# Optimization experiments

Hardware: AMD Instinct MI355X
Metric: run time of the kernel (lower is better)

## Reference

```python
import jax, jax.numpy as jnp
import numpy as np

N_STATE = 2048
N_HEAD = 16
HEAD_DIM = N_STATE // N_HEAD  # 128
ROPE_THETA = 10000.0


def setup_inputs() -> dict:
    key = jax.random.key(0)
    ks = jax.random.split(key, 8)
    B, S, D = 2, 2048, N_STATE
    scale = 1.0 / np.sqrt(D)
    x = jax.random.normal(ks[0], (B, S, D), dtype=jnp.float32)
    Wq = jax.random.normal(ks[1], (D, D), dtype=jnp.float32) * scale
    bq = jnp.zeros((D,), dtype=jnp.float32)
    Wk = jax.random.normal(ks[2], (D, D), dtype=jnp.float32) * scale  # key has no bias
    Wv = jax.random.normal(ks[3], (D, D), dtype=jnp.float32) * scale
    bv = jnp.zeros((D,), dtype=jnp.float32)
    Wo = jax.random.normal(ks[4], (D, D), dtype=jnp.float32) * scale
    bo = jnp.zeros((D,), dtype=jnp.float32)
    return {"x": x, "Wq": Wq, "bq": bq, "Wk": Wk, "Wv": Wv, "bv": bv, "Wo": Wo, "bo": bo}


def _rope(t, pos):
    # t: [B, S, H, hd]; torchtune-style interleaved rotary (pairs of adjacent dims)
    hd = t.shape[-1]
    inv_freq = 1.0 / (ROPE_THETA ** (jnp.arange(0, hd, 2, dtype=jnp.float32) / hd))  # [hd/2]
    ang = pos[:, None] * inv_freq[None, :]                    # [S, hd/2]
    cos = jnp.cos(ang)[None, :, None, :].astype(t.dtype)       # [1,S,1,hd/2]
    sin = jnp.sin(ang)[None, :, None, :].astype(t.dtype)
    t1 = t[..., 0::2]
    t2 = t[..., 1::2]
    rot = jnp.stack([t1 * cos - t2 * sin, t2 * cos + t1 * sin], axis=-1)
    return rot.reshape(t.shape)


def reference(x, Wq, bq, Wk, Wv, bv, Wo, bo):
    B, S, D = x.shape
    H, hd = N_HEAD, D // N_HEAD
    q = (x @ Wq.T + bq).reshape(B, S, H, hd)
    k = (x @ Wk.T).reshape(B, S, H, hd)
    v = (x @ Wv.T + bv).reshape(B, S, H, hd)
    pos = jnp.arange(S, dtype=jnp.float32)
    q = _rope(q, pos)
    k = _rope(k, pos)
    # [B,H,S,hd]
    q = q.transpose(0, 2, 1, 3)
    k = k.transpose(0, 2, 1, 3)
    v = v.transpose(0, 2, 1, 3)
    scale = 1.0 / jnp.sqrt(jnp.asarray(hd, dtype=x.dtype))
    scores = jnp.einsum('bhqd,bhkd->bhqk', q, k) * scale       # [B,H,S,S]
    causal = jnp.tril(jnp.ones((S, S), dtype=bool))
    scores = jnp.where(causal[None, None], scores, jnp.finfo(scores.dtype).min)
    probs = jax.nn.softmax(scores, axis=-1)
    a = jnp.einsum('bhqk,bhkd->bhqd', probs, v)                # [B,H,S,hd]
    a = a.transpose(0, 2, 1, 3).reshape(B, S, D)
    return a @ Wo.T + bo
```

## Files before the change

kernel.cpp:

```cpp
#include <hip/hip_runtime.h>
#include <stdint.h>

typedef float f32x4 __attribute__((ext_vector_type(4)));
typedef __bf16 bf16x8 __attribute__((ext_vector_type(8)));
typedef unsigned short us8 __attribute__((ext_vector_type(8)));
typedef unsigned short us4 __attribute__((ext_vector_type(4)));
typedef unsigned int u32;

#define MFMA16(A, B, C) __builtin_amdgcn_mfma_f32_16x16x32_bf16( \
    __builtin_bit_cast(bf16x8, (A)), __builtin_bit_cast(bf16x8, (B)), (C), 0, 0, 0)

__device__ __forceinline__ unsigned short f2bf(float f) {
  u32 u = __builtin_bit_cast(u32, f);
  u = u + 0x7fffu + ((u >> 16) & 1u);
  return (unsigned short)(u >> 16);
}
__device__ __forceinline__ float bf2f(unsigned short b) {
  u32 u = ((u32)b) << 16;
  return __builtin_bit_cast(float, u);
}
__device__ __forceinline__ void gload16(const void* g, void* lds) {
  __builtin_amdgcn_global_load_lds((const __attribute__((address_space(1))) u32*)g,
                                   (__attribute__((address_space(3))) u32*)lds, 16, 0, 0);
}

__global__ __launch_bounds__(256) void convert_all(
    const float* __restrict__ x, const float* __restrict__ wq, const float* __restrict__ wk,
    const float* __restrict__ wv, const float* __restrict__ wo,
    unsigned short* __restrict__ xb, unsigned short* __restrict__ wcat,
    unsigned short* __restrict__ wob, float2* __restrict__ tab) {
  if (blockIdx.x >= 2048) {
    int t0 = ((int)blockIdx.x - 2048) * 2048 + (int)threadIdx.x * 8;
#pragma unroll
    for (int j = 0; j < 8; ++j) {
      int idx = t0 + j;
      int s = idx >> 6, i = idx & 63;
      float ang = (float)s * exp2f(-(float)i * 0.2076205059304703f);
      float sv, cv;
      sincosf(ang, &sv, &cv);
      tab[idx] = make_float2(cv, sv);
    }
    return;
  }
  int tid = blockIdx.x * 256 + threadIdx.x;
  int nth = 2048 * 256;
  const float* srcs[5] = {x, wq, wk, wv, wo};
  unsigned short* dsts[5] = {xb, wcat, wcat + 4194304, wcat + 8388608, wob};
  const int n4s[5] = {2097152, 1048576, 1048576, 1048576, 1048576};
#pragma unroll
  for (int sg = 0; sg < 5; ++sg) {
    const float4* s = (const float4*)srcs[sg];
    us4* d = (us4*)dsts[sg];
    int n4 = n4s[sg];
    for (int i = tid; i < n4; i += nth) {
      float4 v = s[i];
      us4 o;
      o[0] = f2bf(v.x); o[1] = f2bf(v.y); o[2] = f2bf(v.z); o[3] = f2bf(v.w);
      d[i] = o;
    }
  }
}

template <int EPI>
__global__ __launch_bounds__(512, 2) void gemmsw(
    const unsigned short* __restrict__ A, const unsigned short* __restrict__ B,
    int nTN, int N,
    float* __restrict__ outF, const float* __restrict__ bias,
    unsigned short* __restrict__ qb, unsigned short* __restrict__ kb,
    unsigned short* __restrict__ vtb, const float* __restrict__ bq,
    const float* __restrict__ bv, const float2* __restrict__ tab) {
  constexpr int KT = 32;
  __shared__ alignas(16) char L[131072];
  char* Lp = L;
  int bid = (int)blockIdx.x, nwg = (int)gridDim.x;
  {
    int qq = nwg >> 3;
    int xcd = bid & 7, idx = bid >> 3;
    bid = xcd * qq + idx;
  }
  int tm = bid / nTN, tn = bid % nTN;
  int t = (int)threadIdx.x, l = t & 63, w = t >> 6;
  int g = l >> 4, ln = l & 15;
  int wr = w >> 2, wc = w & 3;
  int lr = l >> 3, lc = l & 7;
  int scol = lc ^ lr;
  const unsigned short* pAs = A + (size_t)(tm * 256 + w * 8 + lr) * 2048 + scol * 8;
  const unsigned short* pBs = B + (size_t)(tn * 256 + w * 8 + lr) * 2048 + scol * 8;

  f32x4 acc[2][2][4][2] = {};
  us8 af[4][2], bf[2][2][2];

#define FENCE asm volatile("" ::: "memory")
#define BAR do { FENCE; __builtin_amdgcn_s_barrier(); FENCE; } while (0)
#define VMW_(n) asm volatile("s_waitcnt vmcnt(" #n ")" ::: "memory")
#define VMW(n) VMW_(n)
#define STA(i, kt, bufsel) do { if ((kt) < KT)                                \
    gload16(pAs + (size_t)(i) * 131072 + (size_t)(kt) * 64,                   \
            Lp + (bufsel) * 65536 + (i) * 8192 + w * 1024); } while (0)
#define STB(i, kt, bufsel) do { if ((kt) < KT)                                \
    gload16(pBs + (size_t)(i) * 131072 + (size_t)(kt) * 64,                   \
            Lp + (bufsel) * 65536 + 32768 + (i) * 8192 + w * 1024); } while (0)
#define RD_A(mh_, bufsel) do {                                                \
    _Pragma("unroll") for (int mf = 0; mf < 4; ++mf)                          \
    _Pragma("unroll") for (int kc = 0; kc < 2; ++kc)                          \
      af[mf][kc] = *(const us8*)(Lp + (bufsel) * 65536 +                      \
          (wr * 128 + (mh_) * 64 + mf * 16 + ln) * 128 +                      \
          ((kc * 64 + g * 16) ^ ((ln & 7) << 4)));                            \
  } while (0)
#define RD_B(nh_, bufsel) do {                                                \
    _Pragma("unroll") for (int nf = 0; nf < 2; ++nf)                          \
    _Pragma("unroll") for (int kc = 0; kc < 2; ++kc)                          \
      bf[nh_][nf][kc] = *(const us8*)(Lp + (bufsel) * 65536 + 32768 +         \
          (wc * 64 + (nh_) * 32 + nf * 16 + ln) * 128 +                       \
          ((kc * 64 + g * 16) ^ ((ln & 7) << 4)));                            \
  } while (0)
#define MM(mh_, nh_) do {                                                     \
    __builtin_amdgcn_s_setprio(1);                                            \
    _Pragma("unroll") for (int mf = 0; mf < 4; ++mf)                          \
    _Pragma("unroll") for (int nf = 0; nf < 2; ++nf)                          \
    _Pragma("unroll") for (int kc = 0; kc < 2; ++kc)                          \
      acc[mh_][nh_][mf][nf] = MFMA16(af[mf][kc], bf[nh_][nf][kc],             \
                                     acc[mh_][nh_][mf][nf]);                  \
    __builtin_amdgcn_s_setprio(0);                                            \
  } while (0)
#define TILE(kt, b, VM0, VM1, VM3) do {                                       \
   RD_A(0, b); RD_B(0, b);                                             \
          STB(0, (kt) + 1, (b) ^ 1); STB(1, (kt) + 1, (b) ^ 1);               \
          BAR; MM(0, 0); VMW(VM0); BAR;                                       \
   RD_B(1, b);                                                         \
          STA(0, (kt) + 1, (b) ^ 1); STA(2, (kt) + 1, (b) ^ 1);               \
          BAR; MM(0, 1); VMW(VM1); BAR;                                       \
   RD_A(1, b);                                                         \
          STB(2, (kt) + 1, (b) ^ 1); STB(3, (kt) + 1, (b) ^ 1);               \
          BAR; MM(1, 0); BAR;                                                 \
   STA(1, (kt) + 1, (b) ^ 1); STA(3, (kt) + 1, (b) ^ 1);               \
          MM(1, 1); VMW(VM3); BAR;                                            \
} while (0)

  STB(0, 0, 0); STB(1, 0, 0); STA(0, 0, 0); STA(2, 0, 0);
  STB(2, 0, 0); STB(3, 0, 0); STA(1, 0, 0); STA(3, 0, 0);
  VMW(4); BAR;

#pragma unroll 1
  for (int kt = 0; kt < 30; kt += 2) {
    TILE(kt, 0, 4, 4, 4);
    TILE(kt + 1, 1, 4, 4, 4);
  }
  TILE(30, 0, 4, 4, 4);
  TILE(31, 1, 2, 0, 0);

#undef TILE
#undef MM
#undef RD_B
#undef RD_A
#undef STB
#undef STA
#undef VMW
#undef VMW_
#undef BAR
#undef FENCE

  if (EPI == 1) {
#pragma unroll
    for (int mh = 0; mh < 2; ++mh)
#pragma unroll
    for (int nh = 0; nh < 2; ++nh)
#pragma unroll
    for (int mf = 0; mf < 4; ++mf)
#pragma unroll
    for (int nf = 0; nf < 2; ++nf) {
      int n = tn * 256 + wc * 64 + nh * 32 + nf * 16 + ln;
      float bz = bias[n];
      int m0 = tm * 256 + wr * 128 + mh * 64 + mf * 16 + g * 4;
#pragma unroll
      for (int r = 0; r < 4; ++r)
        outF[(size_t)(m0 + r) * N + n] = acc[mh][nh][mf][nf][r] + bz;
    }
  } else {
#pragma unroll
    for (int mh = 0; mh < 2; ++mh)
#pragma unroll
    for (int nh = 0; nh < 2; ++nh)
#pragma unroll
    for (int mf = 0; mf < 4; ++mf)
#pragma unroll
    for (int nf = 0; nf < 2; ++nf) {
      int n6 = tn * 256 + wc * 64 + nh * 32 + nf * 16 + ln;
      int sel = n6 >> 11, d = n6 & 2047, h = d >> 7, hd = d & 127;
      int m0 = tm * 256 + wr * 128 + mh * 64 + mf * 16 + g * 4;
      int b = m0 >> 11, s0 = m0 & 2047;
      if (sel == 2) {
        float badd = bv[d];
        us4 pk;
#pragma unroll
        for (int r = 0; r < 4; ++r) pk[r] = f2bf(acc[mh][nh][mf][nf][r] + badd);
        *(us4*)&vtb[((size_t)(b * 16 + h) * 128 + hd) * 2048 + s0] = pk;
      } else {
        unsigned short* dst = sel ? kb : qb;
        float badd = sel ? 0.f : bq[d];
        int odd = hd & 1;
#pragma unroll
        for (int r = 0; r < 4; ++r) {
          float val = acc[mh][nh][mf][nf][r] + badd;
          float pv = __shfl_xor(val, 1);
          float2 cs = tab[((s0 + r) << 6) | (hd >> 1)];
          float rot = odd ? (val * cs.x + pv * cs.y) : (val * cs.x - pv * cs.y);
          dst[((size_t)(b * 16 + h) * 2048 + (s0 + r)) * 128 + hd] = f2bf(rot);
        }
      }
    }
  }
}

template <int EPI>
__global__ __launch_bounds__(512, 2) void gemm2(
    const unsigned short* __restrict__ A, const unsigned short* __restrict__ B,
    int nTN, int N,
    float* __restrict__ outF, const float* __restrict__ bias) {
  constexpr int K = 2048, KT = 64;
  __shared__ alignas(16) char L[4 * 24576];
  int bid = (int)blockIdx.x, nwg = (int)gridDim.x;
  {
    int qq = nwg >> 3;
    int xcd = bid & 7, idx = bid >> 3;
    bid = xcd * qq + idx;
  }
  int tm = bid / nTN, tn = bid % nTN;
  int t = (int)threadIdx.x, l = t & 63, w = t >> 6;
  int g = l >> 4, ln = l & 15;
  int wr = w >> 2, wc = w & 3;
  const unsigned short* Ab =
      A + (size_t)(tm * 128 + w * 16 + (l >> 2)) * K + (((l & 3) ^ ((l >> 4) & 3))) * 8;
  const unsigned short* Bb =
      B + (size_t)(tn * 256 + w * 16 + (l >> 2)) * K + (((l & 3) ^ ((l >> 4) & 3))) * 8;
  f32x4 acc[4][4] = {};

#define STAGE(tile) do {                                                      \
    char* Lb = L + ((tile) & 3) * 24576 + w * 1024;                           \
    int kc = (tile) * 32;                                                     \
    gload16(Ab + kc, Lb);                                                     \
    gload16(Bb + kc, Lb + 8192);                                              \
    gload16(Bb + (size_t)128 * K + kc, Lb + 16384);                           \
  } while (0)

#define GITER(kt, VM) do {                                                    \
    asm volatile("s_waitcnt vmcnt(" #VM ")" ::: "memory");                    \
    __builtin_amdgcn_s_barrier();                                             \
    __builtin_amdgcn_sched_barrier(0);                                        \
    asm volatile("" ::: "memory");                                            \
    if ((kt) + 3 < KT) STAGE((kt) + 3);                                       \
    const unsigned short* Lc = (const unsigned short*)(L + ((kt) & 3) * 24576); \
    us8 af[4], bfr[4];                                                        \
    _Pragma("unroll") for (int mf = 0; mf < 4; ++mf)                          \
      af[mf] = *(const us8*)&Lc[(wr * 64 + mf * 16 + ln) * 32 +               \
                                ((g ^ ((ln >> 2) & 3)) * 8)];                 \
    _Pragma("unroll") for (int nf = 0; nf < 4; ++nf)                          \
      bfr[nf] = *(const us8*)&Lc[4096 + (wc * 64 + nf * 16 + ln) * 32 +       \
                                 ((g ^ ((ln >> 2) & 3)) * 8)];                \
    __builtin_amdgcn_s_setprio(1);                                            \
    _Pragma("unroll") for (int mf = 0; mf < 4; ++mf)                          \
      _Pragma("unroll") for (int nf = 0; nf < 4; ++nf)                        \
        acc[mf][nf] = MFMA16(af[mf], bfr[nf], acc[mf][nf]);                   \
    __builtin_amdgcn_s_setprio(0);                                            \
  } while (0)

  STAGE(0); STAGE(1); STAGE(2);
#pragma unroll 1
  for (int kt = 0; kt < KT - 2; ++kt) GITER(kt, 6);
  GITER(KT - 2, 3);
  GITER(KT - 1, 0);
#undef STAGE
#undef GITER

#pragma unroll
  for (int mf = 0; mf < 4; ++mf)
#pragma unroll
    for (int nf = 0; nf < 4; ++nf) {
      int n = tn * 256 + wc * 64 + nf * 16 + ln;
      float bz = bias[n];
#pragma unroll
      for (int r = 0; r < 4; ++r) {
        int m = tm * 128 + wr * 64 + mf * 16 + g * 4 + r;
        outF[(size_t)m * N + n] = acc[mf][nf][r] + bz;
      }
    }
}

__global__ __launch_bounds__(512) void attn_k(
    const unsigned short* __restrict__ qg, const unsigned short* __restrict__ kg,
    const unsigned short* __restrict__ vtg, unsigned short* __restrict__ ab) {
  __shared__ alignas(16) unsigned short Kl[64 * 128];
  __shared__ alignas(16) unsigned short Vl[128 * 64];
  __shared__ alignas(16) unsigned short Pl[8][16 * 72];
  int bh = (int)blockIdx.x & 31;
  int pr = (int)blockIdx.x >> 5;
  int t = (int)threadIdx.x, l = t & 63, w = t >> 6;
  int g = l >> 4, ln = l & 15;
  int b = bh >> 4, h = bh & 15;
  const size_t bq0 = (size_t)bh * 2048 * 128;

#pragma unroll 1
  for (int half = 0; half < 2; ++half) {
    int qt = half ? 15 - pr : pr;
    int qbase = qt * 128;
    int qrow = qbase + w * 16 + ln;
    us8 qf[4];
#pragma unroll
    for (int kf = 0; kf < 4; ++kf)
      qf[kf] = *(const us8*)&qg[bq0 + (size_t)qrow * 128 + kf * 32 + g * 8];
    f32x4 o[8] = {};
    float mrow = -1e30f, lrow = 0.f;
    int nkt = (qbase >> 6) + 2;
#pragma unroll 1
    for (int kt = 0; kt < nkt; ++kt) {
      __syncthreads();
#pragma unroll
      for (int i = 0; i < 2; ++i) {
        int fb = i * 8192 + w * 1024;
        int flat = fb + l * 16;
        int row = flat >> 8, colb = flat & 255;
        int sc = colb ^ ((row & 7) << 4);
        gload16(kg + (bq0 + (size_t)(kt * 64 + row) * 128 + (sc >> 1)), (char*)Kl + fb);
        int rv = flat >> 7, cv2 = flat & 127;
        int scv = cv2 ^ ((rv & 7) << 4);
        gload16(vtg + (bq0 + (size_t)rv * 2048 + kt * 64 + (scv >> 1)), (char*)Vl + fb);
      }
      __syncthreads();
      f32x4 st[4];
#pragma unroll
      for (int kfr = 0; kfr < 4; ++kfr) {
        f32x4 acc = {};
        int row = kfr * 16 + ln;
        int swz = (row & 7) << 4;
#pragma unroll
        for (int kf = 0; kf < 4; ++kf) {
          us8 kfrag = *(const us8*)((const char*)Kl + row * 256 + ((kf * 64 + g * 16) ^ swz));
          acc = MFMA16(kfrag, qf[kf], acc);
        }
        st[kfr] = acc;
      }
      float pmax = -1e30f;
#pragma unroll
      for (int kfr = 0; kfr < 4; ++kfr)
#pragma unroll
        for (int r = 0; r < 4; ++r) {
          int key = kt * 64 + kfr * 16 + g * 4 + r;
          float sv = key <= qrow ? st[kfr][r] * 0.08838834764831845f : -1e30f;
          st[kfr][r] = sv;
          pmax = fmaxf(pmax, sv);
        }
      pmax = fmaxf(pmax, __shfl_xor(pmax, 16));
      pmax = fmaxf(pmax, __shfl_xor(pmax, 32));
      if (__ballot(pmax > mrow + 8.f)) {
        float mnew = pmax > mrow + 8.f ? pmax : mrow;
        float corr = exp2f((mrow - mnew) * 1.44269504f);
        mrow = mnew;
        lrow *= corr;
#pragma unroll
        for (int r = 0; r < 4; ++r) {
          float cr = __shfl(corr, g * 4 + r);
#pragma unroll
          for (int nf = 0; nf < 8; ++nf) o[nf][r] *= cr;
        }
      }
      float lsum = 0.f;
#pragma unroll
      for (int kfr = 0; kfr < 4; ++kfr) {
        us4 pk;
#pragma unroll
        for (int r = 0; r < 4; ++r) {
          float p = exp2f((st[kfr][r] - mrow) * 1.44269504f);
          lsum += p;
          pk[r] = f2bf(p);
        }
        *(us4*)&Pl[w][ln * 72 + kfr * 16 + g * 4] = pk;
      }
      lsum += __shfl_xor(lsum, 16);
      lsum += __shfl_xor(lsum, 32);
      lrow += lsum;
#pragma unroll
      for (int kf2 = 0; kf2 < 2; ++kf2) {
        us8 pa = *(const us8*)&Pl[w][ln * 72 + kf2 * 32 + g * 8];
#pragma unroll
        for (int nf = 0; nf < 8; ++nf) {
          int row = nf * 16 + ln;
          us8 vb = *(const us8*)((const char*)Vl + row * 128 +
                                 ((kf2 * 64 + g * 16) ^ ((row & 7) << 4)));
          o[nf] = MFMA16(pa, vb, o[nf]);
        }
      }
    }
    float invl = 1.f / lrow;
#pragma unroll
    for (int r = 0; r < 4; ++r) {
      float ir = __shfl(invl, g * 4 + r);
      int srow = qbase + w * 16 + g * 4 + r;
      size_t base = ((size_t)b * 2048 + srow) * 2048 + h * 128 + ln;
#pragma unroll
      for (int nf = 0; nf < 8; ++nf) ab[base + (size_t)nf * 16] = f2bf(o[nf][r] * ir);
    }
  }
}

extern "C" void kernel_launch(void* const* d_in, const int* in_sizes, int n_in,
                              void* d_out, int out_size, void* d_ws, size_t ws_size,
                              hipStream_t stream) {
  const float* x  = (const float*)d_in[0];
  const float* Wq = (const float*)d_in[1];
  const float* bq = (const float*)d_in[2];
  const float* Wk = (const float*)d_in[3];
  const float* Wv = (const float*)d_in[4];
  const float* bv = (const float*)d_in[5];
  const float* Wo = (const float*)d_in[6];
  const float* bo = (const float*)d_in[7];
  float* out = (float*)d_out;

  unsigned short* ws = (unsigned short*)d_ws;
  unsigned short* xb   = ws;
  unsigned short* wcat = xb + 8388608;
  unsigned short* wob  = wcat + 12582912;
  unsigned short* qb   = wob + 4194304;
  unsigned short* kb   = qb + 8388608;
  unsigned short* vtb  = kb + 8388608;
  float2* tab = (float2*)(vtb + 8388608);

  convert_all<<<2112, 256, 0, stream>>>(x, Wq, Wk, Wv, Wo, xb, wcat, wob, tab);
  gemmsw<0><<<384, 512, 0, stream>>>(xb, wcat, 24, 6144,
                                     nullptr, nullptr, qb, kb, vtb, bq, bv, tab);
  attn_k<<<256, 512, 0, stream>>>(qb, kb, vtb, xb );
  gemm2<1><<<256, 512, 0, stream>>>(xb, wob, 8, 2048, out, bo);
}
```

Before: 267.0 us.

## Process paired query tiles together sharing double-buffered K/V tiles in attention

The attention kernel now handles its two causal query tiles (the early and the late one) in the same key loop instead of one after the other. Each K/V tile staged in LDS is used by both tiles, so the shared prefix of keys is loaded only once. K/V staging is also double-buffered: the next tile is prefetched while the current one is computed, which leaves one barrier per iteration instead of two. In exchange, two sets of output accumulators and Q fragments stay live, which raises register pressure and risks spills at 512 threads per block, and the LDS footprint grows.

```diff
diff --git a/kernel.cpp b/kernel.cpp
--- a/kernel.cpp
+++ b/kernel.cpp
@@ -289,8 +289,8 @@
 __global__ __launch_bounds__(512) void attn_k(
     const unsigned short* __restrict__ qg, const unsigned short* __restrict__ kg,
     const unsigned short* __restrict__ vtg, unsigned short* __restrict__ ab) {
-  __shared__ alignas(16) unsigned short Kl[64 * 128];
-  __shared__ alignas(16) unsigned short Vl[128 * 64];
+  __shared__ alignas(16) unsigned short Kl[2][64 * 128];
+  __shared__ alignas(16) unsigned short Vl[2][128 * 64];
   __shared__ alignas(16) unsigned short Pl[8][16 * 72];
   int bh = (int)blockIdx.x & 31;
   int pr = (int)blockIdx.x >> 5;
@@ -299,105 +299,123 @@
   int b = bh >> 4, h = bh & 15;
   const size_t bq0 = (size_t)bh * 2048 * 128;
 
+  const int qbA = pr * 128, qbB = (15 - pr) * 128;
+  const int qrowA = qbA + w * 16 + ln, qrowB = qbB + w * 16 + ln;
+  us8 qfA[4], qfB[4];
+#pragma unroll
+  for (int kf = 0; kf < 4; ++kf) {
+    qfA[kf] = *(const us8*)&qg[bq0 + (size_t)qrowA * 128 + kf * 32 + g * 8];
+    qfB[kf] = *(const us8*)&qg[bq0 + (size_t)qrowB * 128 + kf * 32 + g * 8];
+  }
+  f32x4 oA[8] = {}, oB[8] = {};
+  float mA = -1e30f, lA = 0.f, mB = -1e30f, lB = 0.f;
+  const int nktA = (qbA >> 6) + 2;
+  const int nkt  = (qbB >> 6) + 2;
+
+#define STAGEKV(kt1, bsel) do {                                               \
+    _Pragma("unroll") for (int i = 0; i < 2; ++i) {                           \
+      int fb = i * 8192 + w * 1024;                                           \
+      int flat = fb + l * 16;                                                 \
+      int row = flat >> 8, colb = flat & 255;                                 \
+      int sc = colb ^ ((row & 7) << 4);                                       \
+      gload16(kg + (bq0 + (size_t)((kt1) * 64 + row) * 128 + (sc >> 1)),      \
+              (char*)Kl + (bsel) * 16384 + fb);                               \
+      int rv = flat >> 7, cv2 = flat & 127;                                   \
+      int scv = cv2 ^ ((rv & 7) << 4);                                        \
+      gload16(vtg + (bq0 + (size_t)rv * 2048 + (kt1) * 64 + (scv >> 1)),      \
+              (char*)Vl + (bsel) * 16384 + fb);                               \
+    }                                                                         \
+  } while (0)
+
+#define COMPUTE(qf, o, mrow, lrow, qrow, kt, bo) do {                         \
+    f32x4 st[4];                                                              \
+    _Pragma("unroll") for (int kfr = 0; kfr < 4; ++kfr) {                     \
+      f32x4 acc = {};                                                         \
+      int row = kfr * 16 + ln;                                                \
+      int swz = (row & 7) << 4;                                               \
+      _Pragma("unroll") for (int kf = 0; kf < 4; ++kf) {                      \
+        us8 kfrag = *(const us8*)((const char*)Kl + (bo) + row * 256 +        \
+                                  ((kf * 64 + g * 16) ^ swz));                \
+        acc = MFMA16(kfrag, qf[kf], acc);                                     \
+      }                                                                       \
+      st[kfr] = acc;                                                          \
+    }                                                                         \
+    float pmax = -1e30f;                                                      \
+    _Pragma("unroll") for (int kfr = 0; kfr < 4; ++kfr)                       \
+    _Pragma("unroll") for (int r = 0; r < 4; ++r) {                           \
+      int key = (kt) * 64 + kfr * 16 + g * 4 + r;                             \
+      float sv = key <= (qrow) ? st[kfr][r] * 0.08838834764831845f : -1e30f;  \
+      st[kfr][r] = sv;                                                        \
+      pmax = fmaxf(pmax, sv);                                                 \
+    }                                                                         \
+    pmax = fmaxf(pmax, __shfl_xor(pmax, 16));                                 \
+    pmax = fmaxf(pmax, __shfl_xor(pmax, 32));                                 \
+    if (__ballot(pmax > (mrow) + 8.f)) {                                      \
+      float mnew = pmax > (mrow) + 8.f ? pmax : (mrow);                       \
+      float corr = exp2f(((mrow) - mnew) * 1.44269504f);                      \
+      (mrow) = mnew;                                                          \
+      (lrow) *= corr;                                                         \
+      _Pragma("unroll") for (int r = 0; r < 4; ++r) {                         \
+        float cr = __shfl(corr, g * 4 + r);                                   \
+        _Pragma("unroll") for (int nf = 0; nf < 8; ++nf) o[nf][r] *= cr;      \
+      }                                                                       \
+    }                                                                         \
+    float lsum = 0.f;                                                         \
+    _Pragma("unroll") for (int kfr = 0; kfr < 4; ++kfr) {                     \
+      us4 pk;                                                                 \
+      _Pragma("unroll") for (int r = 0; r < 4; ++r) {                         \
+        float p = exp2f((st[kfr][r] - (mrow)) * 1.44269504f);                 \
+        lsum += p;                                                            \
+        pk[r] = f2bf(p);                                                      \
+      }                                                                       \
+      *(us4*)&Pl[w][ln * 72 + kfr * 16 + g * 4] = pk;                         \
+    }                                                                         \
+    lsum += __shfl_xor(lsum, 16);                                             \
+    lsum += __shfl_xor(lsum, 32);                                             \
+    (lrow) += lsum;                                                           \
+    _Pragma("unroll") for (int kf2 = 0; kf2 < 2; ++kf2) {                     \
+      us8 pa = *(const us8*)&Pl[w][ln * 72 + kf2 * 32 + g * 8];               \
+      _Pragma("unroll") for (int nf = 0; nf < 8; ++nf) {                      \
+        int row = nf * 16 + ln;                                               \
+        us8 vb = *(const us8*)((const char*)Vl + (bo) + row * 128 +           \
+                               ((kf2 * 64 + g * 16) ^ ((row & 7) << 4)));     \
+        o[nf] = MFMA16(pa, vb, o[nf]);                                        \
+      }                                                                       \
+    }                                                                         \
+  } while (0)
+
+  STAGEKV(0, 0);
 #pragma unroll 1
-  for (int half = 0; half < 2; ++half) {
-    int qt = half ? 15 - pr : pr;
-    int qbase = qt * 128;
-    int qrow = qbase + w * 16 + ln;
-    us8 qf[4];
-#pragma unroll
-    for (int kf = 0; kf < 4; ++kf)
-      qf[kf] = *(const us8*)&qg[bq0 + (size_t)qrow * 128 + kf * 32 + g * 8];
-    f32x4 o[8] = {};
-    float mrow = -1e30f, lrow = 0.f;
-    int nkt = (qbase >> 6) + 2;
-#pragma unroll 1
-    for (int kt = 0; kt < nkt; ++kt) {
-      __syncthreads();
-#pragma unroll
-      for (int i = 0; i < 2; ++i) {
-        int fb = i * 8192 + w * 1024;
-        int flat = fb + l * 16;
-        int row = flat >> 8, colb = flat & 255;
-        int sc = colb ^ ((row & 7) << 4);
-        gload16(kg + (bq0 + (size_t)(kt * 64 + row) * 128 + (sc >> 1)), (char*)Kl + fb);
-        int rv = flat >> 7, cv2 = flat & 127;
-        int scv = cv2 ^ ((rv & 7) << 4);
-        gload16(vtg + (bq0 + (size_t)rv * 2048 + kt * 64 + (scv >> 1)), (char*)Vl + fb);
-      }
-      __syncthreads();
-      f32x4 st[4];
-#pragma unroll
-      for (int kfr = 0; kfr < 4; ++kfr) {
-        f32x4 acc = {};
-        int row = kfr * 16 + ln;
-        int swz = (row & 7) << 4;
-#pragma unroll
-        for (int kf = 0; kf < 4; ++kf) {
-          us8 kfrag = *(const us8*)((const char*)Kl + row * 256 + ((kf * 64 + g * 16) ^ swz));
-          acc = MFMA16(kfrag, qf[kf], acc);
-        }
-        st[kfr] = acc;
-      }
-      float pmax = -1e30f;
-#pragma unroll
-      for (int kfr = 0; kfr < 4; ++kfr)
-#pragma unroll
-        for (int r = 0; r < 4; ++r) {
-          int key = kt * 64 + kfr * 16 + g * 4 + r;
-          float sv = key <= qrow ? st[kfr][r] * 0.08838834764831845f : -1e30f;
-          st[kfr][r] = sv;
-          pmax = fmaxf(pmax, sv);
-        }
-      pmax = fmaxf(pmax, __shfl_xor(pmax, 16));
-      pmax = fmaxf(pmax, __shfl_xor(pmax, 32));
-      if (__ballot(pmax > mrow + 8.f)) {
-        float mnew = pmax > mrow + 8.f ? pmax : mrow;
-        float corr = exp2f((mrow - mnew) * 1.44269504f);
-        mrow = mnew;
-        lrow *= corr;
-#pragma unroll
-        for (int r = 0; r < 4; ++r) {
-          float cr = __shfl(corr, g * 4 + r);
-#pragma unroll
-          for (int nf = 0; nf < 8; ++nf) o[nf][r] *= cr;
-        }
-      }
-      float lsum = 0.f;
-#pragma unroll
-      for (int kfr = 0; kfr < 4; ++kfr) {
-        us4 pk;
-#pragma unroll
-        for (int r = 0; r < 4; ++r) {
-          float p = exp2f((st[kfr][r] - mrow) * 1.44269504f);
-          lsum += p;
-          pk[r] = f2bf(p);
-        }
-        *(us4*)&Pl[w][ln * 72 + kfr * 16 + g * 4] = pk;
-      }
-      lsum += __shfl_xor(lsum, 16);
-      lsum += __shfl_xor(lsum, 32);
-      lrow += lsum;
-#pragma unroll
-      for (int kf2 = 0; kf2 < 2; ++kf2) {
-        us8 pa = *(const us8*)&Pl[w][ln * 72 + kf2 * 32 + g * 8];
-#pragma unroll
-        for (int nf = 0; nf < 8; ++nf) {
-          int row = nf * 16 + ln;
-          us8 vb = *(const us8*)((const char*)Vl + row * 128 +
-                                 ((kf2 * 64 + g * 16) ^ ((row & 7) << 4)));
-          o[nf] = MFMA16(pa, vb, o[nf]);
-        }
-      }
-    }
-    float invl = 1.f / lrow;
+  for (int kt = 0; kt < nkt; ++kt) {
+    __syncthreads();
+    if (kt + 1 < nkt) STAGEKV(kt + 1, (kt + 1) & 1);
+    int bo = (kt & 1) * 16384;
+    COMPUTE(qfB, oB, mB, lB, qrowB, kt, bo);
+    if (kt < nktA) COMPUTE(qfA, oA, mA, lA, qrowA, kt, bo);
+  }
+#undef COMPUTE
+#undef STAGEKV
+
+  {
+    float invl = 1.f / lB;
 #pragma unroll
     for (int r = 0; r < 4; ++r) {
       float ir = __shfl(invl, g * 4 + r);
-      int srow = qbase + w * 16 + g * 4 + r;
+      int srow = qbB + w * 16 + g * 4 + r;
       size_t base = ((size_t)b * 2048 + srow) * 2048 + h * 128 + ln;
 #pragma unroll
-      for (int nf = 0; nf < 8; ++nf) ab[base + (size_t)nf * 16] = f2bf(o[nf][r] * ir);
+      for (int nf = 0; nf < 8; ++nf) ab[base + (size_t)nf * 16] = f2bf(oB[nf][r] * ir);
+    }
+  }
+  {
+    float invl = 1.f / lA;
+#pragma unroll
+    for (int r = 0; r < 4; ++r) {
+      float ir = __shfl(invl, g * 4 + r);
+      int srow = qbA + w * 16 + g * 4 + r;
+      size_t base = ((size_t)b * 2048 + srow) * 2048 + h * 128 + ln;
+#pragma unroll
+      for (int nf = 0; nf < 8; ++nf) ab[base + (size_t)nf * 16] = f2bf(oA[nf][r] * ir);
     }
   }
 }
```

New measurement: 266.3 us. About the same (-0.2%).
